# Optimization experiments

Hardware: AMD Instinct MI355X
Metric: run time of the kernel (lower is better)

The kernel has to match this reference:

```python
import jax, jax.numpy as jnp
import numpy as np

NUM_HEADS = 16
HEAD_DIM = 64  # 1024 / 16


def setup_inputs() -> dict:
    key = jax.random.key(0)
    ks = jax.random.split(key, 8)
    B, S, D = 2, 2048, 1024
    s = 0.02
    return {
        "hidden_states_q": jax.random.normal(ks[0], (B, S, D), jnp.float32),
        "hidden_states_k": jax.random.normal(ks[1], (B, S, D), jnp.float32),
        "hidden_states_v": jax.random.normal(ks[2], (B, S, D), jnp.float32),
        "Wq": jax.random.normal(ks[3], (D, D), jnp.float32) * s,
        "bq": jnp.zeros((D,), jnp.float32),
        "Wk": jax.random.normal(ks[4], (D, D), jnp.float32) * s,
        "bk": jnp.zeros((D,), jnp.float32),
        "Wv": jax.random.normal(ks[5], (D, D), jnp.float32) * s,
        "bv": jnp.zeros((D,), jnp.float32),
        "Wp": jax.random.normal(ks[6], (D, D), jnp.float32) * s,
        "bp": jnp.zeros((D,), jnp.float32),
    }


def _split_heads(x):
    B, S, D = x.shape
    return x.reshape(B, S, NUM_HEADS, HEAD_DIM).transpose(0, 2, 1, 3)  # [B,H,S,dh]


def reference(hidden_states_q, hidden_states_k, hidden_states_v,
              Wq, bq, Wk, bk, Wv, bv, Wp, bp):
    # Projections (Linear / Conv1D are both x @ W + b in this parameterization)
    q = _split_heads(hidden_states_q @ Wq + bq)
    k = _split_heads(hidden_states_k @ Wk + bk)
    v = _split_heads(hidden_states_v @ Wv + bv)
    scale = 1.0 / jnp.sqrt(jnp.asarray(HEAD_DIM, q.dtype))
    # NOTE: no causal mask is applied in the original _attn (mask asserted None)
    attn = jnp.einsum("bhqd,bhkd->bhqk", q, k) * scale
    attn = jax.nn.softmax(attn, axis=-1)  # attn_dropout is identity in eval
    out = jnp.einsum("bhqk,bhkd->bhqd", attn, v)
    B, H, S, dh = out.shape
    out = out.transpose(0, 2, 1, 3).reshape(B, S, H * dh)
    out = out @ Wp + bp  # resid_dropout identity in eval
    return out
```

## Files before the change

kernel.cpp:

```cpp
#include <hip/hip_runtime.h>
#include <stdint.h>


typedef _Float16 f16;
typedef __attribute__((ext_vector_type(8))) _Float16 f16x8;
typedef __attribute__((ext_vector_type(4))) _Float16 f16x4;
typedef __attribute__((ext_vector_type(2))) _Float16 f16x2;
typedef __attribute__((ext_vector_type(4))) float f32x4;
typedef __attribute__((ext_vector_type(16))) float f32x16;
typedef __attribute__((ext_vector_type(2))) unsigned u32x2;

#define NB 2
#define SEQ 2048
#define DMODEL 1024
#define NH 16
#define DH 64

#define QSCALE 0.1803368801111601f

__device__ __forceinline__ void gload_lds16(const void* g, void* l) {
  __builtin_amdgcn_global_load_lds(
      (const __attribute__((address_space(1))) unsigned int*)g,
      (__attribute__((address_space(3))) unsigned int*)l, 16, 0, 0);
}

__device__ __forceinline__ void plswap(unsigned& a, unsigned& b) {
  u32x2 r = __builtin_amdgcn_permlane32_swap(a, b, false, false);
  a = r[0];
  b = r[1];
}

__global__ __launch_bounds__(256) void prep(
    const float* __restrict__ hq, const float* __restrict__ hk,
    const float* __restrict__ hv, f16* __restrict__ xq, f16* __restrict__ xk,
    f16* __restrict__ xv, const float* __restrict__ w0,
    const float* __restrict__ w1, const float* __restrict__ w2,
    const float* __restrict__ w3, f16* __restrict__ t0, f16* __restrict__ t1,
    f16* __restrict__ t2, f16* __restrict__ t3) {
  __shared__ float tile[64][65];
  const int z = blockIdx.z;
  if (z < 3) {
    const float* src = z == 0 ? hq : (z == 1 ? hk : hv);
    f16* dst = z == 0 ? xq : (z == 1 ? xk : xv);
    int i = (blockIdx.x * 256 + threadIdx.x) * 8;
    float4 a = *(const float4*)(src + i);
    float4 b = *(const float4*)(src + i + 4);
    f16x8 o;
    o[0] = (f16)a.x; o[1] = (f16)a.y; o[2] = (f16)a.z; o[3] = (f16)a.w;
    o[4] = (f16)b.x; o[5] = (f16)b.y; o[6] = (f16)b.z; o[7] = (f16)b.w;
    *(f16x8*)(dst + i) = o;
    return;
  }
  if (blockIdx.x >= 256) return;
  const float* W; f16* T;
  switch (z - 3) {
    case 0: W = w0; T = t0; break;
    case 1: W = w1; T = t1; break;
    case 2: W = w2; T = t2; break;
    default: W = w3; T = t3; break;
  }
  int r0 = (blockIdx.x >> 4) * 64, c0 = (blockIdx.x & 15) * 64;
  for (int it = 0; it < 16; ++it) {
    int idx = it * 256 + threadIdx.x;
    int r = idx >> 6, c = idx & 63;
    tile[r][c] = W[(size_t)(r0 + r) * DMODEL + c0 + c];
  }
  __syncthreads();
  for (int it = 0; it < 16; ++it) {
    int idx = it * 256 + threadIdx.x;
    int r = idx >> 6, c = idx & 63;
    T[(size_t)(c0 + r) * DMODEL + r0 + c] = (f16)tile[c][r];
  }
}

__global__ __launch_bounds__(256) void gemm128(
    const f16* __restrict__ xq, const f16* __restrict__ xk,
    const f16* __restrict__ xv,
    const f16* __restrict__ wqt, const f16* __restrict__ wkt,
    const f16* __restrict__ wvt,
    const float* __restrict__ bq, const float* __restrict__ bk,
    const float* __restrict__ bv,
    f16* __restrict__ qo, f16* __restrict__ ko, f16* __restrict__ vto) {
  __shared__ char lds[32768];
  char* ldsA = lds;
  char* ldsB = lds + 16384;

  int mode = blockIdx.z;
  const f16* Am; const f16* Bt; const float* bias; float oscale = 1.0f;
  if (mode == 0)      { Am = xq; Bt = wqt; bias = bq; oscale = QSCALE; }
  else if (mode == 1) { Am = xk; Bt = wkt; bias = bk; }
  else                { Am = xv; Bt = wvt; bias = bv; }

  const int tid = threadIdx.x;
  const int l = tid & 63, w = tid >> 6;
  const int g = l >> 4, c = l & 15;
  const int wr = w >> 1, wc = w & 1;
  const int m0 = blockIdx.y * 128, n0 = blockIdx.x * 128;

  const int srow = w * 8 + (l >> 3);
  const int schunk = (l & 7) ^ ((l >> 3) & 7);

  f32x4 acc[4][4] = {};

  for (int k0 = 0; k0 < DMODEL; k0 += 64) {
#pragma unroll
    for (int it = 0; it < 4; ++it) {
      int row = it * 32 + srow;
      gload_lds16(Am + (size_t)(m0 + row) * DMODEL + k0 + schunk * 8,
                  ldsA + it * 4096 + w * 1024);
    }
#pragma unroll
    for (int it = 0; it < 4; ++it) {
      int row = it * 32 + srow;
      gload_lds16(Bt + (size_t)(n0 + row) * DMODEL + k0 + schunk * 8,
                  ldsB + it * 4096 + w * 1024);
    }
    __syncthreads();
    f16x8 af[2][4], bf[2][4];
#pragma unroll
    for (int kc = 0; kc < 2; ++kc)
#pragma unroll
      for (int i = 0; i < 4; ++i) {
        int row = wr * 64 + i * 16 + c;
        af[kc][i] = *(const f16x8*)(ldsA + row * 128 + (((kc * 4 + g) ^ (row & 7)) << 4));
        int rowb = wc * 64 + i * 16 + c;
        bf[kc][i] = *(const f16x8*)(ldsB + rowb * 128 + (((kc * 4 + g) ^ (rowb & 7)) << 4));
      }
#pragma unroll
    for (int kc = 0; kc < 2; ++kc)
#pragma unroll
      for (int i = 0; i < 4; ++i)
#pragma unroll
        for (int j = 0; j < 4; ++j)
          acc[i][j] = __builtin_amdgcn_mfma_f32_16x16x32_f16(af[kc][i], bf[kc][j],
                                                             acc[i][j], 0, 0, 0);
    __syncthreads();
  }

#pragma unroll
  for (int i = 0; i < 4; ++i) {
#pragma unroll
    for (int j = 0; j < 4; ++j) {
      int grb = m0 + wr * 64 + i * 16 + g * 4;
      int gc = n0 + wc * 64 + j * 16 + c;
      float bval = bias[gc];
      if (mode == 2) {
        int b = grb >> 11, s = grb & 2047, h = gc >> 6, d = gc & 63;
        f16x4 pk;
#pragma unroll
        for (int e = 0; e < 4; ++e) pk[e] = (f16)(acc[i][j][e] + bval);
        *(f16x4*)(vto + ((size_t)((b * NH + h) * DH + d)) * SEQ + s) = pk;
      } else {
        f16* dst = (mode == 0) ? qo : ko;
        int b = grb >> 11, s = grb & 2047, h = gc >> 6, d = gc & 63;
#pragma unroll
        for (int e = 0; e < 4; ++e)
          dst[(((size_t)(b * NH + h) * SEQ) + (s + e)) * DH + d] =
              (f16)((acc[i][j][e] + bval) * oscale);
      }
    }
  }
}

__global__ __launch_bounds__(256) void gemm_out(
    const f16* __restrict__ ao, const f16* __restrict__ wpt,
    const float* __restrict__ bp, float* __restrict__ out) {
  __shared__ char lds[24576];
  char* ldsA = lds;
  char* ldsB = lds + 16384;

  const int tid = threadIdx.x;
  const int l = tid & 63, w = tid >> 6;
  const int g = l >> 4, c = l & 15;
  const int wr = w >> 1, wc = w & 1;
  const int m0 = blockIdx.y * 128, n0 = blockIdx.x * 64;

  const int srow = w * 8 + (l >> 3);
  const int schunk = (l & 7) ^ ((l >> 3) & 7);

  f32x4 acc[4][2] = {};

  for (int k0 = 0; k0 < DMODEL; k0 += 64) {
#pragma unroll
    for (int it = 0; it < 4; ++it) {
      int row = it * 32 + srow;
      gload_lds16(ao + (size_t)(m0 + row) * DMODEL + k0 + schunk * 8,
                  ldsA + it * 4096 + w * 1024);
    }
#pragma unroll
    for (int it = 0; it < 2; ++it) {
      int row = it * 32 + srow;
      gload_lds16(wpt + (size_t)(n0 + row) * DMODEL + k0 + schunk * 8,
                  ldsB + it * 4096 + w * 1024);
    }
    __syncthreads();
    f16x8 af[2][4], bf[2][2];
#pragma unroll
    for (int kc = 0; kc < 2; ++kc) {
#pragma unroll
      for (int i = 0; i < 4; ++i) {
        int row = wr * 64 + i * 16 + c;
        af[kc][i] = *(const f16x8*)(ldsA + row * 128 + (((kc * 4 + g) ^ (row & 7)) << 4));
      }
#pragma unroll
      for (int j = 0; j < 2; ++j) {
        int rowb = wc * 32 + j * 16 + c;
        bf[kc][j] = *(const f16x8*)(ldsB + rowb * 128 + (((kc * 4 + g) ^ (rowb & 7)) << 4));
      }
    }
#pragma unroll
    for (int kc = 0; kc < 2; ++kc)
#pragma unroll
      for (int i = 0; i < 4; ++i)
#pragma unroll
        for (int j = 0; j < 2; ++j)
          acc[i][j] = __builtin_amdgcn_mfma_f32_16x16x32_f16(af[kc][i], bf[kc][j],
                                                             acc[i][j], 0, 0, 0);
    __syncthreads();
  }

#pragma unroll
  for (int i = 0; i < 4; ++i)
#pragma unroll
    for (int j = 0; j < 2; ++j) {
      int grb = m0 + wr * 64 + i * 16 + g * 4;
      int gc = n0 + wc * 32 + j * 16 + c;
      float bval = bp[gc];
#pragma unroll
      for (int e = 0; e < 4; ++e)
        out[(size_t)(grb + e) * DMODEL + gc] = acc[i][j][e] + bval;
    }
}

__global__ __launch_bounds__(256, 2) void attn64(
    const f16* __restrict__ qg, const f16* __restrict__ kg,
    const f16* __restrict__ vtg, f16* __restrict__ aout) {
  __shared__ char lds[33792];

  const int tid = threadIdx.x;
  const int l = tid & 63, w = tid >> 6;
  const int q31 = l & 31;
  const bool hi = l >= 32;
  const int p = w & 1;
  const int qgrp = w >> 1;

  const int bid = blockIdx.x;
  const int bh = (bid & 7) + 8 * (bid >> 7);
  const int qc = (bid >> 3) & 15;
  const int q0 = qc * 128 + qgrp * 64;

  f16x8 qf0[4], qf1[4];
#pragma unroll
  for (int ks = 0; ks < 4; ++ks) {
    qf0[ks] = *(const f16x8*)(qg + ((size_t)bh * SEQ + q0 + q31) * DH + ks * 16 +
                              (hi ? 8 : 0));
    qf1[ks] = *(const f16x8*)(qg + ((size_t)bh * SEQ + q0 + 32 + q31) * DH +
                              ks * 16 + (hi ? 8 : 0));
  }

  float lsum0 = 0.0f, lsum1 = 0.0f;
  f32x16 oacc00 = {}, oacc01 = {}, oacc10 = {}, oacc11 = {};

  const int srow = w * 8 + (l >> 3);
  const int schunk = (l & 7) ^ ((l >> 3) & 7);

  auto stage = [&](int buf, int t) {
    char* baseK = lds + buf * 16384;
    char* baseV = baseK + 8192;
#pragma unroll
    for (int it = 0; it < 2; ++it) {
      int row = it * 32 + srow;
      gload_lds16(kg + ((size_t)bh * SEQ + t * 64 + row) * DH + schunk * 8,
                  baseK + it * 4096 + w * 1024);
      gload_lds16(vtg + ((size_t)bh * DH + row) * SEQ + t * 64 + schunk * 8,
                  baseV + it * 4096 + w * 1024);
    }
  };

  const f16x2 one2 = {(f16)1.0f, (f16)1.0f};

  auto softmax = [&](const f32x16& st, float& lsum, unsigned* dw) {
    float ps[16];
#pragma unroll
    for (int r = 0; r < 16; ++r) ps[r] = exp2f(st[r]);
#pragma unroll
    for (int i = 0; i < 8; ++i)
      dw[i] = __builtin_bit_cast(
          unsigned, __builtin_amdgcn_cvt_pkrtz(ps[2 * i], ps[2 * i + 1]));
    float sA = 0.0f, sB = 0.0f;
#pragma unroll
    for (int i = 0; i < 4; ++i) {
      sA = __builtin_amdgcn_fdot2(__builtin_bit_cast(f16x2, dw[i]), one2, sA, false);
      sB = __builtin_amdgcn_fdot2(__builtin_bit_cast(f16x2, dw[4 + i]), one2, sB, false);
    }
    lsum += sA + sB;
    plswap(dw[0], dw[2]);
    plswap(dw[1], dw[3]);
    plswap(dw[4], dw[6]);
    plswap(dw[5], dw[7]);
  };

  stage(0, 0);

  for (int t = 0; t < 32; ++t) {
    int cur = t & 1;
    if (t + 1 < 32) {
      stage(cur ^ 1, t + 1);
      asm volatile("s_waitcnt vmcnt(4)" ::: "memory");
    } else {
      asm volatile("s_waitcnt vmcnt(0)" ::: "memory");
    }
    __builtin_amdgcn_s_barrier();
    __builtin_amdgcn_sched_barrier(0);

    const char* ldsK = lds + cur * 16384;
    const char* ldsV = ldsK + 8192;

    f32x16 st0 = {}, st1 = {};
#pragma unroll
    for (int ks = 0; ks < 4; ++ks) {
      int row = p * 32 + q31;
      int ch = ((ks * 2 + (hi ? 1 : 0)) ^ (q31 & 7)) << 4;
      f16x8 kf = *(const f16x8*)(ldsK + row * 128 + ch);
      st0 = __builtin_amdgcn_mfma_f32_32x32x16_f16(kf, qf0[ks], st0, 0, 0, 0);
      st1 = __builtin_amdgcn_mfma_f32_32x32x16_f16(kf, qf1[ks], st1, 0, 0, 0);
    }

    unsigned dw0[8], dw1[8];
    softmax(st0, lsum0, dw0);
    softmax(st1, lsum1, dw1);

#pragma unroll
    for (int ks2 = 0; ks2 < 2; ++ks2) {
      union { unsigned u[4]; f16x8 v; } pb0, pb1;
      pb0.u[0] = dw0[ks2 * 4 + 0]; pb0.u[1] = dw0[ks2 * 4 + 1];
      pb0.u[2] = dw0[ks2 * 4 + 2]; pb0.u[3] = dw0[ks2 * 4 + 3];
      pb1.u[0] = dw1[ks2 * 4 + 0]; pb1.u[1] = dw1[ks2 * 4 + 1];
      pb1.u[2] = dw1[ks2 * 4 + 2]; pb1.u[3] = dw1[ks2 * 4 + 3];
      {
        int vrow = q31;
        int ch = ((p * 4 + ks2 * 2 + (hi ? 1 : 0)) ^ (vrow & 7)) << 4;
        f16x8 vf = *(const f16x8*)(ldsV + vrow * 128 + ch);
        oacc00 = __builtin_amdgcn_mfma_f32_32x32x16_f16(vf, pb0.v, oacc00, 0, 0, 0);
        oacc10 = __builtin_amdgcn_mfma_f32_32x32x16_f16(vf, pb1.v, oacc10, 0, 0, 0);
      }
      {
        int vrow = 32 + q31;
        int ch = ((p * 4 + ks2 * 2 + (hi ? 1 : 0)) ^ (vrow & 7)) << 4;
        f16x8 vf = *(const f16x8*)(ldsV + vrow * 128 + ch);
        oacc01 = __builtin_amdgcn_mfma_f32_32x32x16_f16(vf, pb0.v, oacc01, 0, 0, 0);
        oacc11 = __builtin_amdgcn_mfma_f32_32x32x16_f16(vf, pb1.v, oacc11, 0, 0, 0);
      }
    }
    __builtin_amdgcn_sched_barrier(0);
    __builtin_amdgcn_s_barrier();
  }

  __builtin_amdgcn_s_barrier();
  char* reg = lds + qgrp * 16896;
  if (p == 1) {
#pragma unroll
    for (int j = 0; j < 8; ++j) {
      f32x4 c0, c1;
#pragma unroll
      for (int e = 0; e < 4; ++e) {
        c0[e] = (j < 4) ? oacc00[j * 4 + e] : oacc01[(j - 4) * 4 + e];
        c1[e] = (j < 4) ? oacc10[j * 4 + e] : oacc11[(j - 4) * 4 + e];
      }
      *(f32x4*)(reg + j * 1024 + l * 16) = c0;
      *(f32x4*)(reg + 8192 + j * 1024 + l * 16) = c1;
    }
    *(float*)(reg + 16384 + l * 4) = lsum0;
    *(float*)(reg + 16640 + l * 4) = lsum1;
  }
  __syncthreads();
  if (p == 0) {
#pragma unroll
    for (int j = 0; j < 8; ++j) {
      f32x4 c0 = *(const f32x4*)(reg + j * 1024 + l * 16);
      f32x4 c1 = *(const f32x4*)(reg + 8192 + j * 1024 + l * 16);
#pragma unroll
      for (int e = 0; e < 4; ++e) {
        if (j < 4) { oacc00[j * 4 + e] += c0[e]; oacc10[j * 4 + e] += c1[e]; }
        else       { oacc01[(j - 4) * 4 + e] += c0[e]; oacc11[(j - 4) * 4 + e] += c1[e]; }
      }
    }
    float lt0 = lsum0 + *(const float*)(reg + 16384 + l * 4);
    float lt1 = lsum1 + *(const float*)(reg + 16640 + l * 4);
    lt0 += __shfl_xor(lt0, 32);
    lt1 += __shfl_xor(lt1, 32);
    float inv0 = 1.0f / lt0, inv1 = 1.0f / lt1;
    const int b = bh >> 4, h = bh & 15;
#pragma unroll
    for (int f = 0; f < 2; ++f) {
      float inv = f ? inv1 : inv0;
      int s = q0 + f * 32 + q31;
#pragma unroll
      for (int dt = 0; dt < 2; ++dt)
#pragma unroll
        for (int rg = 0; rg < 4; ++rg) {
          f16x4 pk;
#pragma unroll
          for (int j = 0; j < 4; ++j) {
            float v = f ? (dt ? oacc11[rg * 4 + j] : oacc10[rg * 4 + j])
                        : (dt ? oacc01[rg * 4 + j] : oacc00[rg * 4 + j]);
            pk[j] = (f16)(v * inv);
          }
          int d0 = dt * 32 + rg * 8 + (hi ? 4 : 0);
          *(f16x4*)(aout + ((size_t)(b * SEQ + s)) * DMODEL + h * DH + d0) = pk;
        }
    }
  }
}

extern "C" void kernel_launch(void* const* d_in, const int* in_sizes, int n_in,
                              void* d_out, int out_size, void* d_ws, size_t ws_size,
                              hipStream_t stream) {
  const float* hq = (const float*)d_in[0];
  const float* hk = (const float*)d_in[1];
  const float* hv = (const float*)d_in[2];
  const float* Wq = (const float*)d_in[3];
  const float* bq = (const float*)d_in[4];
  const float* Wk = (const float*)d_in[5];
  const float* bk = (const float*)d_in[6];
  const float* Wv = (const float*)d_in[7];
  const float* bv = (const float*)d_in[8];
  const float* Wp = (const float*)d_in[9];
  const float* bp = (const float*)d_in[10];
  float* out = (float*)d_out;

  f16* xq  = (f16*)d_ws;
  f16* xk  = xq + 4194304;
  f16* xv  = xk + 4194304;
  f16* wqt = xv + 4194304;
  f16* wkt = wqt + 1048576;
  f16* wvt = wkt + 1048576;
  f16* wpt = wvt + 1048576;
  f16* qb  = wpt + 1048576;
  f16* kb  = qb + 4194304;
  f16* vtb = kb + 4194304;
  f16* ao  = vtb + 4194304;

  prep<<<dim3(2048, 1, 7), 256, 0, stream>>>(hq, hk, hv, xq, xk, xv,
                                             Wq, Wk, Wv, Wp, wqt, wkt, wvt, wpt);
  gemm128<<<dim3(8, 32, 3), 256, 0, stream>>>(xq, xk, xv, wqt, wkt, wvt,
                                              bq, bk, bv, qb, kb, vtb);
  attn64<<<dim3(512), 256, 0, stream>>>(qb, kb, vtb, ao);
  gemm_out<<<dim3(16, 32), 256, 0, stream>>>(ao, wpt, bp, out);
}
```

Baseline: 142.7 us.

## Deepen attention K/V pipeline to four LDS stages and remap GEMM block indices

The attention kernel goes from a double-buffered K/V LDS pipeline to a four-stage ring of 64KB, issuing three tiles ahead. The loop drops its trailing barrier in favour of vmcnt-based waits, so global load latency is hidden further ahead. The projection and output GEMMs switch to a 1D grid with a remapped block order that groups M tiles, aiming for better L2 locality across XCDs. The larger LDS footprint may cut attention occupancy below the two blocks per CU requested by launch bounds.

Result: faster. 127.4 us (-10.7%).

```diff
diff --git a/kernel.cpp b/kernel.cpp
--- a/kernel.cpp
+++ b/kernel.cpp
@@ -85,7 +85,12 @@
   char* ldsA = lds;
   char* ldsB = lds + 16384;
 
-  int mode = blockIdx.z;
+  const int bid = blockIdx.x;
+  const int mode = bid >> 8;
+  const int lin = bid & 255;
+  const int m0 = ((lin & 7) + 8 * ((lin >> 3) & 3)) * 128;
+  const int n0 = (lin >> 5) * 128;
+
   const f16* Am; const f16* Bt; const float* bias; float oscale = 1.0f;
   if (mode == 0)      { Am = xq; Bt = wqt; bias = bq; oscale = QSCALE; }
   else if (mode == 1) { Am = xk; Bt = wkt; bias = bk; }
@@ -95,7 +100,6 @@
   const int l = tid & 63, w = tid >> 6;
   const int g = l >> 4, c = l & 15;
   const int wr = w >> 1, wc = w & 1;
-  const int m0 = blockIdx.y * 128, n0 = blockIdx.x * 128;
 
   const int srow = w * 8 + (l >> 3);
   const int schunk = (l & 7) ^ ((l >> 3) & 7);
@@ -169,11 +173,14 @@
   char* ldsA = lds;
   char* ldsB = lds + 16384;
 
+  const int lin = blockIdx.x;
+  const int m0 = ((lin & 7) + 8 * ((lin >> 3) & 3)) * 128;
+  const int n0 = (lin >> 5) * 64;
+
   const int tid = threadIdx.x;
   const int l = tid & 63, w = tid >> 6;
   const int g = l >> 4, c = l & 15;
   const int wr = w >> 1, wc = w & 1;
-  const int m0 = blockIdx.y * 128, n0 = blockIdx.x * 64;
 
   const int srow = w * 8 + (l >> 3);
   const int schunk = (l & 7) ^ ((l >> 3) & 7);
@@ -235,7 +242,7 @@
 __global__ __launch_bounds__(256, 2) void attn64(
     const f16* __restrict__ qg, const f16* __restrict__ kg,
     const f16* __restrict__ vtg, f16* __restrict__ aout) {
-  __shared__ char lds[33792];
+  __shared__ char lds[65536];
 
   const int tid = threadIdx.x;
   const int l = tid & 63, w = tid >> 6;
@@ -300,22 +307,8 @@
     plswap(dw[5], dw[7]);
   };
 
-  stage(0, 0);
-
-  for (int t = 0; t < 32; ++t) {
-    int cur = t & 1;
-    if (t + 1 < 32) {
-      stage(cur ^ 1, t + 1);
-      asm volatile("s_waitcnt vmcnt(4)" ::: "memory");
-    } else {
-      asm volatile("s_waitcnt vmcnt(0)" ::: "memory");
-    }
-    __builtin_amdgcn_s_barrier();
-    __builtin_amdgcn_sched_barrier(0);
-
-    const char* ldsK = lds + cur * 16384;
+  auto compute = [&](const char* ldsK) {
     const char* ldsV = ldsK + 8192;
-
     f32x16 st0 = {}, st1 = {};
 #pragma unroll
     for (int ks = 0; ks < 4; ++ks) {
@@ -325,11 +318,9 @@
       st0 = __builtin_amdgcn_mfma_f32_32x32x16_f16(kf, qf0[ks], st0, 0, 0, 0);
       st1 = __builtin_amdgcn_mfma_f32_32x32x16_f16(kf, qf1[ks], st1, 0, 0, 0);
     }
-
     unsigned dw0[8], dw1[8];
     softmax(st0, lsum0, dw0);
     softmax(st1, lsum1, dw1);
-
 #pragma unroll
     for (int ks2 = 0; ks2 < 2; ++ks2) {
       union { unsigned u[4]; f16x8 v; } pb0, pb1;
@@ -352,11 +343,41 @@
         oacc11 = __builtin_amdgcn_mfma_f32_32x32x16_f16(vf, pb1.v, oacc11, 0, 0, 0);
       }
     }
+  };
+
+  stage(0, 0);
+  stage(1, 1);
+  stage(2, 2);
+
+  asm volatile("s_waitcnt vmcnt(8)" ::: "memory");
+  __builtin_amdgcn_s_barrier();
+  __builtin_amdgcn_sched_barrier(0);
+  stage(3, 3);
+  compute(lds);
+
+#pragma unroll 4
+  for (int t = 1; t <= 28; ++t) {
+    asm volatile("s_waitcnt vmcnt(8)" ::: "memory");
+    __builtin_amdgcn_s_barrier();
     __builtin_amdgcn_sched_barrier(0);
-    __builtin_amdgcn_s_barrier();
-  }
-
+    stage((t + 3) & 3, t + 3);
+    compute(lds + (t & 3) * 16384);
+  }
+
+  asm volatile("s_waitcnt vmcnt(8)" ::: "memory");
   __builtin_amdgcn_s_barrier();
+  __builtin_amdgcn_sched_barrier(0);
+  compute(lds + 1 * 16384);
+  asm volatile("s_waitcnt vmcnt(4)" ::: "memory");
+  __builtin_amdgcn_s_barrier();
+  __builtin_amdgcn_sched_barrier(0);
+  compute(lds + 2 * 16384);
+  asm volatile("s_waitcnt vmcnt(0)" ::: "memory");
+  __builtin_amdgcn_s_barrier();
+  __builtin_amdgcn_sched_barrier(0);
+  compute(lds + 3 * 16384);
+
+  __syncthreads();
   char* reg = lds + qgrp * 16896;
   if (p == 1) {
 #pragma unroll
@@ -443,8 +464,8 @@
 
   prep<<<dim3(2048, 1, 7), 256, 0, stream>>>(hq, hk, hv, xq, xk, xv,
                                              Wq, Wk, Wv, Wp, wqt, wkt, wvt, wpt);
-  gemm128<<<dim3(8, 32, 3), 256, 0, stream>>>(xq, xk, xv, wqt, wkt, wvt,
-                                              bq, bk, bv, qb, kb, vtb);
+  gemm128<<<dim3(768), 256, 0, stream>>>(xq, xk, xv, wqt, wkt, wvt,
+                                         bq, bk, bv, qb, kb, vtb);
   attn64<<<dim3(512), 256, 0, stream>>>(qb, kb, vtb, ao);
-  gemm_out<<<dim3(16, 32), 256, 0, stream>>>(ao, wpt, bp, out);
-}
+  gemm_out<<<dim3(512), 256, 0, stream>>>(ao, wpt, bp, out);
+}
```
